# Kernel optimization log

Measured on AMD Instinct MI355X. Metric: run time of the kernel, lower is better.

The kernel has to match this reference:

```python
import jax, jax.numpy as jnp
import numpy as np

N, E = 50000, 1_000_000
IN_F, OUT_F = 128, 64
NEG_SLOPE = 0.2


def setup_inputs() -> dict:
    key = jax.random.key(0)
    k1, k2, k3, k4, k5 = jax.random.split(key, 5)
    x = jax.random.normal(k1, (N, IN_F), dtype=jnp.float32)
    edge_index = jax.random.randint(k2, (2, E), 0, N, dtype=jnp.int64)
    # xavier_uniform with gain=1.414 (as in the torch init)
    gain = 1.414
    bW = gain * np.sqrt(6.0 / (IN_F + OUT_F))
    W = jax.random.uniform(k3, (IN_F, OUT_F), jnp.float32, -bW, bW)
    ba = gain * np.sqrt(6.0 / (OUT_F + 1))
    a_src = jax.random.uniform(k4, (OUT_F, 1), jnp.float32, -ba, ba)
    a_dst = jax.random.uniform(k5, (OUT_F, 1), jnp.float32, -ba, ba)
    return {"x": x, "edge_index": edge_index, "W": W, "a_src": a_src, "a_dst": a_dst}


def reference(x, edge_index, W, a_src, a_dst):
    n = x.shape[0]
    Wh = x @ W                                  # [N, F_out]
    src = edge_index[0]
    dst = edge_index[1]
    # per-edge attention logits: (Wh[src] . a_src) + (Wh[dst] . a_dst)
    s_src = Wh @ a_src[:, 0]                    # [N]
    s_dst = Wh @ a_dst[:, 0]                    # [N]
    e = jax.nn.leaky_relu(s_src[src] + s_dst[dst], negative_slope=NEG_SLOPE)  # [E]
    e = jnp.exp(e - jnp.max(e))                 # global-max stabilized exp (matches torch code)
    denom = jax.ops.segment_sum(e, dst, num_segments=n) + 1e-16  # [N]
    alpha = e / denom[dst]                      # [E]  (dropout p=0 -> identity)
    out = jax.ops.segment_sum(Wh[src] * alpha[:, None], dst, num_segments=n)  # [N, F_out]
    return jax.nn.elu(out)
```

## Files before the change

kernel.cpp:

```cpp
#include <hip/hip_runtime.h>
#include <hip/hip_bf16.h>
#include <math.h>

#define NN 50000
#define NE 1000000
#define FIN 128
#define FOUT 64
#define NEG 0.2f

#define NB   2048
#define DPB  25
#define NBUSED 2000
#define TS   4096
#define NT   245
#define NTP  256
#define GEMM_BLKS 782

using short8  = __attribute__((ext_vector_type(8))) short;
using floatx4 = __attribute__((ext_vector_type(4))) float;

static __device__ __forceinline__ short f2bf(float f) {
    __hip_bfloat16 h = __float2bfloat16(f);
    return *(short*)&h;
}

__global__ __launch_bounds__(256) void k_front(
    const float* __restrict__ x, const float* __restrict__ W,
    const float* __restrict__ a_src, const float* __restrict__ a_dst,
    const int* __restrict__ ei,
    __hip_bfloat16* __restrict__ Whb, float* __restrict__ s_src,
    float* __restrict__ s_dst,
    unsigned* __restrict__ bdata, int* __restrict__ gofs)
{
    __shared__ int cnt[NB];
    __shared__ int cur[NB];
    __shared__ unsigned srt[TS];
    __shared__ int wsum[4];

    const int tid  = threadIdx.x;
    const int lane = tid & 63;
    const int wv   = tid >> 6;

    if (blockIdx.x < GEMM_BLKS) {
        const int col  = lane & 15;
        const int quad = lane >> 4;
        const int strip = blockIdx.x * 4 + wv;
        if (strip >= NN / 16) return;
        const int row0 = strip * 16;

        short8 bfr[4][4];
        #pragma unroll
        for (int kk = 0; kk < 4; ++kk) {
            #pragma unroll
            for (int nt = 0; nt < 4; ++nt) {
                const float* wp = W + (kk * 32 + quad * 8) * FOUT + nt * 16 + col;
                #pragma unroll
                for (int j = 0; j < 8; ++j)
                    bfr[kk][nt][j] = f2bf(wp[j * FOUT]);
            }
        }

        floatx4 acc[4] = {{0.f,0.f,0.f,0.f},{0.f,0.f,0.f,0.f},
                          {0.f,0.f,0.f,0.f},{0.f,0.f,0.f,0.f}};

        const float* xrow = x + (size_t)(row0 + col) * FIN + quad * 8;
        #pragma unroll
        for (int kk = 0; kk < 4; ++kk) {
            const float4 u0 = *(const float4*)(xrow + kk * 32);
            const float4 u1 = *(const float4*)(xrow + kk * 32 + 4);
            short8 af;
            af[0] = f2bf(u0.x); af[1] = f2bf(u0.y);
            af[2] = f2bf(u0.z); af[3] = f2bf(u0.w);
            af[4] = f2bf(u1.x); af[5] = f2bf(u1.y);
            af[6] = f2bf(u1.z); af[7] = f2bf(u1.w);
            #pragma unroll
            for (int nt = 0; nt < 4; ++nt)
                acc[nt] = __builtin_amdgcn_mfma_f32_16x16x32_bf16(
                    af, bfr[kk][nt], acc[nt], 0, 0, 0);
        }

        const float av0 = a_src[col], av1 = a_src[16 + col];
        const float av2 = a_src[32 + col], av3 = a_src[48 + col];
        const float bv0 = a_dst[col], bv1 = a_dst[16 + col];
        const float bv2 = a_dst[32 + col], bv3 = a_dst[48 + col];

        float ps[4], pd[4];
        #pragma unroll
        for (int reg = 0; reg < 4; ++reg) {
            ps[reg] = acc[0][reg] * av0 + acc[1][reg] * av1
                    + acc[2][reg] * av2 + acc[3][reg] * av3;
            pd[reg] = acc[0][reg] * bv0 + acc[1][reg] * bv1
                    + acc[2][reg] * bv2 + acc[3][reg] * bv3;
        }

        #pragma unroll
        for (int nt = 0; nt < 4; ++nt)
            #pragma unroll
            for (int reg = 0; reg < 4; ++reg)
                Whb[(size_t)(row0 + quad * 4 + reg) * FOUT + nt * 16 + col] =
                    __float2bfloat16(acc[nt][reg]);

        #pragma unroll
        for (int off = 1; off < 16; off <<= 1) {
            #pragma unroll
            for (int reg = 0; reg < 4; ++reg) {
                ps[reg] += __shfl_xor(ps[reg], off);
                pd[reg] += __shfl_xor(pd[reg], off);
            }
        }
        if (col == 0) {
            #pragma unroll
            for (int reg = 0; reg < 4; ++reg) {
                s_src[row0 + quad * 4 + reg] = ps[reg];
                s_dst[row0 + quad * 4 + reg] = pd[reg];
            }
        }
        return;
    }

    const int tile = blockIdx.x - GEMM_BLKS;
    const int base = tile * TS;
    const int tcnt = (NE - base < TS) ? (NE - base) : TS;

    for (int i = tid; i < NB; i += 256) cnt[i] = 0;
    __syncthreads();

    unsigned pk[16];
    #pragma unroll
    for (int j = 0; j < 16; ++j) {
        const int i = j * 256 + tid;
        if (i < tcnt) {
            const int e = base + i;
            const unsigned s = (unsigned)__builtin_nontemporal_load(ei + e);
            const unsigned d = (unsigned)__builtin_nontemporal_load(ei + NE + e);
            pk[j] = (s << 16) | d;
            atomicAdd(&cnt[d / DPB], 1);
        } else pk[j] = 0xFFFFFFFFu;
    }
    __syncthreads();

    {
        const int i0 = tid * 8;
        int v[8], s = 0;
        #pragma unroll
        for (int j = 0; j < 8; ++j) { v[j] = cnt[i0 + j]; s += v[j]; }
        int inc = s;
        #pragma unroll
        for (int off = 1; off < 64; off <<= 1) {
            const int t = __shfl_up(inc, off);
            if (lane >= off) inc += t;
        }
        if (lane == 63) wsum[wv] = inc;
        __syncthreads();
        int wb = 0;
        #pragma unroll
        for (int w = 0; w < 3; ++w) if (w < wv) wb += wsum[w];
        int excl = wb + inc - s;
        int g[8];
        #pragma unroll
        for (int j = 0; j < 8; ++j) { cur[i0 + j] = excl; g[j] = excl; excl += v[j]; }
        *(int4*)(gofs + (size_t)tile * NB + i0)     = make_int4(g[0], g[1], g[2], g[3]);
        *(int4*)(gofs + (size_t)tile * NB + i0 + 4) = make_int4(g[4], g[5], g[6], g[7]);
    }
    __syncthreads();

    #pragma unroll
    for (int j = 0; j < 16; ++j) {
        if (pk[j] != 0xFFFFFFFFu) {
            const int b = (int)(pk[j] & 0xffffu) / DPB;
            const int pos = atomicAdd(&cur[b], 1);
            srt[pos] = pk[j];
        }
    }
    __syncthreads();

    for (int i = tid; i < tcnt; i += 256)
        bdata[base + i] = srt[i];
}

__global__ __launch_bounds__(256) void k_transp(
    const int* __restrict__ gofs, int* __restrict__ gofs_t)
{
    __shared__ int tb[32][33];
    const int bi = blockIdx.x & 63;
    const int ti = blockIdx.x >> 6;
    const int r = threadIdx.x >> 5;
    const int c = threadIdx.x & 31;
    for (int rr = r; rr < 32; rr += 8) {
        const int t = ti * 32 + rr;
        tb[rr][c] = (t < NT) ? gofs[(size_t)t * NB + bi * 32 + c] : 0;
    }
    __syncthreads();
    for (int rr = r; rr < 32; rr += 8) {
        const int b = bi * 32 + rr;
        gofs_t[(size_t)b * NTP + ti * 32 + c] = tb[c][rr];
    }
}

__global__ __launch_bounds__(256) void k_sortgather(
    const int* __restrict__ gofs_t, const unsigned* __restrict__ bdata,
    const float* __restrict__ s_src, const float* __restrict__ s_dst,
    const __hip_bfloat16* __restrict__ Whb, float* __restrict__ out)
{
    __shared__ unsigned raw[1024];
    __shared__ unsigned srt[1024];
    __shared__ float evs[1024];
    __shared__ int cnt[32];
    __shared__ int ofs2[33];
    __shared__ int cur[32];
    __shared__ int wsum[4];

    const int b = blockIdx.x;
    const int tid = threadIdx.x;
    const int lane = tid & 63;
    const int wv = tid >> 6;
    const int d0 = b * DPB;

    if (tid < 32) cnt[tid] = 0;

    int c = 0, o = 0;
    if (tid < NT) {
        o = gofs_t[(size_t)b * NTP + tid];
        c = gofs_t[(size_t)(b + 1) * NTP + tid] - o;
    }
    int inc = c;
    #pragma unroll
    for (int off = 1; off < 64; off <<= 1) {
        const int t = __shfl_up(inc, off);
        if (lane >= off) inc += t;
    }
    if (lane == 63) wsum[wv] = inc;
    __syncthreads();
    int wb = 0;
    #pragma unroll
    for (int w = 0; w < 3; ++w) if (w < wv) wb += wsum[w];
    const int segbase = wb + inc - c;
    const int tot = wsum[0] + wsum[1] + wsum[2] + wsum[3];

    for (int k = 0; k < c; ++k)
        raw[segbase + k] = bdata[(size_t)tid * TS + o + k];
    __syncthreads();

    for (int i = tid; i < tot; i += 256)
        atomicAdd(&cnt[(int)(raw[i] & 0xffffu) - d0], 1);
    __syncthreads();

    if (tid < 32) {
        const int cc = (tid < DPB) ? cnt[tid] : 0;
        int in2 = cc;
        #pragma unroll
        for (int off = 1; off < 32; off <<= 1) {
            const int t = __shfl_up(in2, off);
            if (tid >= off) in2 += t;
        }
        ofs2[tid + 1] = in2;
        if (tid == 0) ofs2[0] = 0;
        cur[tid] = in2 - cc;
    }
    __syncthreads();

    for (int i = tid; i < tot; i += 256) {
        const unsigned p = raw[i];
        const int j = (int)(p & 0xffffu) - d0;
        const int pos = atomicAdd(&cur[j], 1);
        srt[pos] = p;
    }
    __syncthreads();

    for (int i = tid; i < tot; i += 256) {
        const unsigned p = srt[i];
        float v = s_src[p >> 16] + s_dst[p & 0xffffu];
        v = (v > 0.f) ? v : NEG * v;
        evs[i] = __expf(v);
    }
    __syncthreads();

    for (int j = wv; j < DPB; j += 4) {
        const int d = d0 + j;
        const int beg = ofs2[j];
        const int end = ofs2[j + 1];
        float acc = 0.f, den = 0.f;
        int i = beg;
        for (; i + 8 <= end; i += 8) {
            int ss[8]; float ee[8], w[8];
            #pragma unroll
            for (int k = 0; k < 8; ++k) {
                ss[k] = (int)(srt[i + k] >> 16);
                ee[k] = evs[i + k];
            }
            #pragma unroll
            for (int k = 0; k < 8; ++k)
                w[k] = __bfloat162float(Whb[(size_t)ss[k] * FOUT + lane]);
            #pragma unroll
            for (int k = 0; k < 8; ++k) {
                acc = fmaf(ee[k], w[k], acc);
                den += ee[k];
            }
        }
        for (; i < end; ++i) {
            const int s0 = (int)(srt[i] >> 16);
            const float e0 = evs[i];
            acc = fmaf(e0, __bfloat162float(Whb[(size_t)s0 * FOUT + lane]), acc);
            den += e0;
        }
        const float r = acc / (den + 1e-16f);
        out[(size_t)d * FOUT + lane] = (r > 0.f) ? r : expm1f(r);
    }
}

extern "C" void kernel_launch(void* const* d_in, const int* in_sizes, int n_in,
                              void* d_out, int out_size, void* d_ws, size_t ws_size,
                              hipStream_t stream)
{
    const float* x     = (const float*)d_in[0];
    const int*   ei    = (const int*)d_in[1];
    const float* W     = (const float*)d_in[2];
    const float* a_src = (const float*)d_in[3];
    const float* a_dst = (const float*)d_in[4];
    float* out = (float*)d_out;

    float* ws    = (float*)d_ws;
    __hip_bfloat16* Whb = (__hip_bfloat16*)ws;
    float* s_src = ws + (size_t)NN * FOUT / 2;
    float* s_dst = s_src + NN;
    int*   gofs  = (int*)(s_dst + NN);
    int*   gofs_t = gofs + (size_t)NT * NB;
    unsigned* bdata = (unsigned*)(gofs_t + (size_t)NB * NTP);

    k_front<<<GEMM_BLKS + NT, 256, 0, stream>>>(x, W, a_src, a_dst, ei,
                                                Whb, s_src, s_dst, bdata, gofs);
    k_transp<<<512, 256, 0, stream>>>(gofs, gofs_t);
    k_sortgather<<<NBUSED, 256, 0, stream>>>(gofs_t, bdata, s_src, s_dst,
                                             Whb, out);
}
```

Measured before the change: 135.7 us.

## Widen front kernel to 512 threads, fuse edge exp into scatter, swizzle block order

The front kernel moves to 512-thread blocks and puts the tile-sort blocks first, ahead of the GEMM blocks, so the long bucketing work starts early. The per-tile prefix scan is adjusted to handle 4 buckets per thread. In the sort-gather kernel, the attention exp is now computed during the scatter step, using s_dst values staged in shared memory for the block's destinations. This removes one pass over the sorted data and one barrier. Block IDs are also swizzled to spread neighbouring destination ranges across the device, at the cost of higher register and LDS pressure per block in the front kernel.

Result: faster. 123.8 us (-8.8%).

```diff
diff --git a/kernel.cpp b/kernel.cpp
--- a/kernel.cpp
+++ b/kernel.cpp
@@ -14,7 +14,8 @@
 #define TS   4096
 #define NT   245
 #define NTP  256
-#define GEMM_BLKS 782
+#define TILE_BLKS 245
+#define GEMM_BLKS 391
 
 using short8  = __attribute__((ext_vector_type(8))) short;
 using floatx4 = __attribute__((ext_vector_type(4))) float;
@@ -24,7 +25,7 @@
     return *(short*)&h;
 }
 
-__global__ __launch_bounds__(256) void k_front(
+__global__ __launch_bounds__(512) void k_front(
     const float* __restrict__ x, const float* __restrict__ W,
     const float* __restrict__ a_src, const float* __restrict__ a_dst,
     const int* __restrict__ ei,
@@ -35,16 +36,16 @@
     __shared__ int cnt[NB];
     __shared__ int cur[NB];
     __shared__ unsigned srt[TS];
-    __shared__ int wsum[4];
+    __shared__ int wsum[8];
 
     const int tid  = threadIdx.x;
     const int lane = tid & 63;
     const int wv   = tid >> 6;
 
-    if (blockIdx.x < GEMM_BLKS) {
+    if (blockIdx.x >= TILE_BLKS) {
         const int col  = lane & 15;
         const int quad = lane >> 4;
-        const int strip = blockIdx.x * 4 + wv;
+        const int strip = (blockIdx.x - TILE_BLKS) * 8 + wv;
         if (strip >= NN / 16) return;
         const int row0 = strip * 16;
 
@@ -118,17 +119,17 @@
         return;
     }
 
-    const int tile = blockIdx.x - GEMM_BLKS;
+    const int tile = blockIdx.x;
     const int base = tile * TS;
     const int tcnt = (NE - base < TS) ? (NE - base) : TS;
 
-    for (int i = tid; i < NB; i += 256) cnt[i] = 0;
-    __syncthreads();
-
-    unsigned pk[16];
+    for (int i = tid; i < NB; i += 512) cnt[i] = 0;
+    __syncthreads();
+
+    unsigned pk[8];
     #pragma unroll
-    for (int j = 0; j < 16; ++j) {
-        const int i = j * 256 + tid;
+    for (int j = 0; j < 8; ++j) {
+        const int i = j * 512 + tid;
         if (i < tcnt) {
             const int e = base + i;
             const unsigned s = (unsigned)__builtin_nontemporal_load(ei + e);
@@ -140,10 +141,10 @@
     __syncthreads();
 
     {
-        const int i0 = tid * 8;
-        int v[8], s = 0;
-        #pragma unroll
-        for (int j = 0; j < 8; ++j) { v[j] = cnt[i0 + j]; s += v[j]; }
+        const int i0 = tid * 4;
+        const int v0 = cnt[i0], v1 = cnt[i0 + 1];
+        const int v2 = cnt[i0 + 2], v3 = cnt[i0 + 3];
+        const int s = v0 + v1 + v2 + v3;
         int inc = s;
         #pragma unroll
         for (int off = 1; off < 64; off <<= 1) {
@@ -154,18 +155,19 @@
         __syncthreads();
         int wb = 0;
         #pragma unroll
-        for (int w = 0; w < 3; ++w) if (w < wv) wb += wsum[w];
-        int excl = wb + inc - s;
-        int g[8];
-        #pragma unroll
-        for (int j = 0; j < 8; ++j) { cur[i0 + j] = excl; g[j] = excl; excl += v[j]; }
-        *(int4*)(gofs + (size_t)tile * NB + i0)     = make_int4(g[0], g[1], g[2], g[3]);
-        *(int4*)(gofs + (size_t)tile * NB + i0 + 4) = make_int4(g[4], g[5], g[6], g[7]);
+        for (int w = 0; w < 7; ++w) if (w < wv) wb += wsum[w];
+        const int excl = wb + inc - s;
+        cur[i0]     = excl;
+        cur[i0 + 1] = excl + v0;
+        cur[i0 + 2] = excl + v0 + v1;
+        cur[i0 + 3] = excl + v0 + v1 + v2;
+        *(int4*)(gofs + (size_t)tile * NB + i0) =
+            make_int4(excl, excl + v0, excl + v0 + v1, excl + v0 + v1 + v2);
     }
     __syncthreads();
 
     #pragma unroll
-    for (int j = 0; j < 16; ++j) {
+    for (int j = 0; j < 8; ++j) {
         if (pk[j] != 0xFFFFFFFFu) {
             const int b = (int)(pk[j] & 0xffffu) / DPB;
             const int pos = atomicAdd(&cur[b], 1);
@@ -174,7 +176,7 @@
     }
     __syncthreads();
 
-    for (int i = tid; i < tcnt; i += 256)
+    for (int i = tid; i < tcnt; i += 512)
         bdata[base + i] = srt[i];
 }
 
@@ -205,18 +207,22 @@
     __shared__ unsigned raw[1024];
     __shared__ unsigned srt[1024];
     __shared__ float evs[1024];
+    __shared__ float sdl[32];
     __shared__ int cnt[32];
     __shared__ int ofs2[33];
     __shared__ int cur[32];
     __shared__ int wsum[4];
 
-    const int b = blockIdx.x;
+    const int b = (blockIdx.x & 7) * (NBUSED / 8) + (blockIdx.x >> 3);
     const int tid = threadIdx.x;
     const int lane = tid & 63;
     const int wv = tid >> 6;
     const int d0 = b * DPB;
 
-    if (tid < 32) cnt[tid] = 0;
+    if (tid < 32) {
+        cnt[tid] = 0;
+        sdl[tid] = (tid < DPB) ? s_dst[d0 + tid] : 0.f;
+    }
 
     int c = 0, o = 0;
     if (tid < NT) {
@@ -264,14 +270,9 @@
         const int j = (int)(p & 0xffffu) - d0;
         const int pos = atomicAdd(&cur[j], 1);
         srt[pos] = p;
-    }
-    __syncthreads();
-
-    for (int i = tid; i < tot; i += 256) {
-        const unsigned p = srt[i];
-        float v = s_src[p >> 16] + s_dst[p & 0xffffu];
+        float v = s_src[p >> 16] + sdl[j];
         v = (v > 0.f) ? v : NEG * v;
-        evs[i] = __expf(v);
+        evs[pos] = __expf(v);
     }
     __syncthreads();
 
@@ -327,8 +328,8 @@
     int*   gofs_t = gofs + (size_t)NT * NB;
     unsigned* bdata = (unsigned*)(gofs_t + (size_t)NB * NTP);
 
-    k_front<<<GEMM_BLKS + NT, 256, 0, stream>>>(x, W, a_src, a_dst, ei,
-                                                Whb, s_src, s_dst, bdata, gofs);
+    k_front<<<TILE_BLKS + GEMM_BLKS, 512, 0, stream>>>(
+        x, W, a_src, a_dst, ei, Whb, s_src, s_dst, bdata, gofs);
     k_transp<<<512, 256, 0, stream>>>(gofs, gofs_t);
     k_sortgather<<<NBUSED, 256, 0, stream>>>(gofs_t, bdata, s_src, s_dst,
                                              Whb, out);
```
